# Performance work log

Measured on AMD Instinct MI355X. Metric: run time of the kernel, lower is better.

## Reference

```python
import jax, jax.numpy as jnp
import numpy as np

GRID = 128
N0 = 262144
CHANNELS = [16, 32, 64, 128, 256]
EPS = 1e-5
OFFS2 = [(dx, dy, dz) for dx in (0, 1) for dy in (0, 1) for dz in (0, 1)]
OFFS3 = [(dx, dy, dz) for dx in (-1, 0, 1) for dy in (-1, 0, 1) for dz in (-1, 0, 1)]


def _keys(c, size):
    return (c[:, 0].astype(np.int64) * size + c[:, 1]) * size + c[:, 2]


def _rulebook(in_coords, out_coords, offsets, size_in, stride):
    # explicit-GEMM rulebook: for each kernel offset, (input_idx, output_idx) pairs,
    # padded to n_out with a validity mask so shapes are static.
    ik = _keys(in_coords, size_in)
    order = np.argsort(ik)
    sk = ik[order]
    K, P = len(offsets), out_coords.shape[0]
    I = np.zeros((K, P), np.int32)
    O = np.zeros((K, P), np.int32)
    M = np.zeros((K, P), bool)
    for k, off in enumerate(offsets):
        nbr = out_coords * stride + np.asarray(off)
        valid = np.all((nbr >= 0) & (nbr < size_in), axis=1)
        nk = _keys(np.clip(nbr, 0, size_in - 1), size_in)
        pos = np.minimum(np.searchsorted(sk, nk), len(sk) - 1)
        found = valid & (sk[pos] == nk)
        cnt = int(found.sum())
        I[k, :cnt] = order[pos[found]]
        O[k, :cnt] = np.nonzero(found)[0]
        M[k, :cnt] = True
    return I, O, M


def setup_inputs() -> dict:
    rng = np.random.RandomState(0)
    flat = rng.choice(GRID ** 3, size=N0, replace=False)
    coords = np.stack([flat // (GRID * GRID), (flat // GRID) % GRID, flat % GRID], 1).astype(np.int64)
    key = jax.random.key(0)
    ctr = [0]
    def nrm(shape, scale=1.0):
        ctr[0] += 1
        return scale * jax.random.normal(jax.random.fold_in(key, ctr[0]), shape, jnp.float32)
    inp = {"x": nrm((N0, CHANNELS[0]))}
    size = GRID
    for l in range(4):
        cin, cout = CHANNELS[l], CHANNELS[l + 1]
        out_coords = np.unique(coords // 2, axis=0)
        dI, dO, dM = _rulebook(coords, out_coords, OFFS2, size, 2)       # stride-2, k=2 down conv
        bI, bO, bM = _rulebook(out_coords, out_coords, OFFS3, size // 2, 1)  # stride-1, k=3 block conv
        inp[f"dW{l}"] = nrm((8, cin, cout), (8 * cin) ** -0.5)
        inp[f"dI{l}"] = jnp.asarray(dI); inp[f"dO{l}"] = jnp.asarray(dO); inp[f"dM{l}"] = jnp.asarray(dM)
        inp[f"dG{l}"] = 1.0 + nrm((cout,), 0.1)
        inp[f"dB{l}"] = nrm((cout,), 0.1)
        inp[f"dN{l}"] = int(out_coords.shape[0])
        inp[f"bW{l}"] = nrm((27, cout, cout), (27 * cout) ** -0.5)
        inp[f"bC{l}"] = nrm((cout,), 0.01)
        inp[f"bI{l}"] = jnp.asarray(bI); inp[f"bO{l}"] = jnp.asarray(bO); inp[f"bM{l}"] = jnp.asarray(bM)
        inp[f"bG{l}"] = 1.0 + nrm((cout,), 0.1)
        inp[f"bH{l}"] = nrm((cout,), 0.1)
        coords = out_coords
        size //= 2
    return inp


def _conv(f, W, I, O, M, n_out, bias=None):
    # gather -> GEMM -> scatter-add, one pass per kernel offset (fixed small K)
    out = jnp.zeros((n_out, W.shape[-1]), f.dtype)
    for k in range(W.shape[0]):
        g = jnp.where(M[k][:, None], f[I[k]], 0.0)
        out = out.at[O[k]].add(g @ W[k])
    return out if bias is None else out + bias


def _bn_relu(f, g, b):
    # training-mode BatchNorm over active voxels, fused with ReLU
    m = f.mean(0)
    v = jnp.mean((f - m) ** 2, 0)
    return jax.nn.relu((f - m) * (g * jax.lax.rsqrt(v + EPS)) + b)


def _forward(x, levels):
    outs = [x]
    for (dW, dI, dO, dM, dG, dB, dN, bW, bC, bI, bO, bM, bG, bH) in levels:
        x = _bn_relu(_conv(x, dW, dI, dO, dM, dN), dG, dB)        # down block (bias=False)
        x = _bn_relu(_conv(x, bW, bI, bO, bM, dN, bC), bG, bH)    # ConvBlock
        outs.append(x)
    return tuple(outs)


def reference(x, dW0, dI0, dO0, dM0, dG0, dB0, dN0, bW0, bC0, bI0, bO0, bM0, bG0, bH0,
              dW1, dI1, dO1, dM1, dG1, dB1, dN1, bW1, bC1, bI1, bO1, bM1, bG1, bH1,
              dW2, dI2, dO2, dM2, dG2, dB2, dN2, bW2, bC2, bI2, bO2, bM2, bG2, bH2,
              dW3, dI3, dO3, dM3, dG3, dB3, dN3, bW3, bC3, bI3, bO3, bM3, bG3, bH3):
    levels = [
        (dW0, dI0, dO0, dM0, dG0, dB0, dN0, bW0, bC0, bI0, bO0, bM0, bG0, bH0),
        (dW1, dI1, dO1, dM1, dG1, dB1, dN1, bW1, bC1, bI1, bO1, bM1, bG1, bH1),
        (dW2, dI2, dO2, dM2, dG2, dB2, dN2, bW2, bC2, bI2, bO2, bM2, bG2, bH2),
        (dW3, dI3, dO3, dM3, dG3, dB3, dN3, bW3, bC3, bI3, bO3, bM3, bG3, bH3),
    ]
    return _forward(x, levels)
```

## Files before the change

kernel.cpp:

```cpp
#include <hip/hip_runtime.h>
#include <hip/hip_bf16.h>
#include <stdint.h>
#include <stddef.h>

typedef __hip_bfloat16 bf16;
typedef __attribute__((ext_vector_type(8))) short bf8_t;
typedef __attribute__((ext_vector_type(4))) float f4_t;
static const int CH[5] = {16, 32, 64, 128, 256};

__device__ __forceinline__ float b2f(unsigned short u) {
    return __uint_as_float(((unsigned int)u) << 16);
}
__device__ __forceinline__ unsigned short f2bu(float f) {
    union { bf16 h; unsigned short u; } cv;
    cv.h = __float2bfloat16(f);
    return cv.u;
}
__device__ __forceinline__ void fma4(float4& a, float s, const float4& w) {
    a.x = fmaf(s, w.x, a.x);
    a.y = fmaf(s, w.y, a.y);
    a.z = fmaf(s, w.z, a.z);
    a.w = fmaf(s, w.w, a.w);
}
struct us4 { unsigned short a, b, c, d; };

__global__ void k_sentinel(float* __restrict__ out, float v) {
    if (threadIdx.x == 0) out[0] = v;
}

__global__ void SparseConvEncoder_20633022890309_kernel(
        const unsigned char* __restrict__ bM0, int* __restrict__ flag) {
    if (threadIdx.x == 0) {
        flag[0] = 1;
        flag[1] = 0;
        flag[2] = (bM0[0] == 1 && bM0[1] == 0 && bM0[2] == 0 && bM0[3] == 0 && bM0[4] == 1) ? 1 : 0;
    }
}

__global__ void __launch_bounds__(256) k_copy(const float* __restrict__ x,
                                              float* __restrict__ y, long n) {
    long i = (long)blockIdx.x * 256 + threadIdx.x;
    if (i < n) y[i] = x[i];
}

__global__ void __launch_bounds__(256) k_tob(const float* __restrict__ x,
                                             unsigned short* __restrict__ y, long n) {
    long i = (long)blockIdx.x * 256 + threadIdx.x;
    if (i < n) y[i] = f2bu(x[i]);
}

__global__ void __launch_bounds__(256) k_wt(const float* __restrict__ W,
                                            unsigned short* __restrict__ Wt,
                                            int cin, int cout, long tot) {
    long i = (long)blockIdx.x * 256 + threadIdx.x;
    if (i >= tot) return;
    long cc = (long)cin * cout;
    int k = (int)(i / cc);
    int rem = (int)(i % cc);
    int co = rem / cin, ci = rem % cin;
    Wt[i] = f2bu(W[((long)k * cin + ci) * cout + co]);
}

__global__ void __launch_bounds__(256) k_scatter(const int* __restrict__ I,
                                                 const int* __restrict__ O,
                                                 const void* __restrict__ M,
                                                 const int* __restrict__ flag,
                                                 int* __restrict__ R, int P, int k0, int cnt) {
    int i = blockIdx.x * 256 + threadIdx.x;
    if (i >= cnt) return;
    long gi = (long)k0 * P + i;
    int m = flag[2] ? ((const int*)M)[gi] : (int)((const unsigned char*)M)[gi];
    if (!m) return;
    R[(long)(i / P) * P + O[gi]] = I[gi];
}

__global__ void __launch_bounds__(256) k_init(float* __restrict__ out,
                                              const float* __restrict__ bias,
                                              long total, int maskC) {
    long i = (long)blockIdx.x * 256 + threadIdx.x;
    if (i < total) out[i] = bias ? bias[i & maskC] : 0.f;
}

template <int CIN, int TN, int MODE>
__global__ void __launch_bounds__(256) k_mconv(const unsigned short* __restrict__ Xb,
                                               const unsigned short* __restrict__ Wt,
                                               const float* __restrict__ bias,
                                               const int* __restrict__ R,
                                               float* __restrict__ out,
                                               int n, int cout, int kcnt, int gs) {
    const int lane = threadIdx.x & 63;
    const int wave = threadIdx.x >> 6;
    const int rt = blockIdx.x * 4 + wave;
    const int row_tiles = (n + 15) >> 4;
    if (rt >= row_tiles) return;
    const int m = lane & 15, q = lane >> 4;
    const int o = rt * 16 + m;
    const int co0 = blockIdx.y * (16 * TN);
    const bf8_t zero = {};

    f4_t acc[TN];
#pragma unroll
    for (int t = 0; t < TN; ++t) {
        if (MODE == 0) {
            float bv = bias ? bias[co0 + t * 16 + m] : 0.f;
            acc[t][0] = bv; acc[t][1] = bv; acc[t][2] = bv; acc[t][3] = bv;
        } else if (MODE == 1) {
#pragma unroll
            for (int g = 0; g < 4; ++g) {
                int row = rt * 16 + q * 4 + g;
                acc[t][g] = (row < n) ? out[(long)row * cout + co0 + t * 16 + m] : 0.f;
            }
        } else {
            acc[t][0] = 0.f; acc[t][1] = 0.f; acc[t][2] = 0.f; acc[t][3] = 0.f;
        }
    }

    int ks = 0, ke = kcnt;
    if (MODE == 2) {
        ks = blockIdx.z * gs;
        ke = ks + gs;
        if (ke > kcnt) ke = kcnt;
    }

    bool touched = false;
    for (int kk = ks; kk < ke; ++kk) {
        int r = (o < n) ? R[(long)kk * n + o] : -1;
        if (__ballot(r >= 0) == 0ULL) continue;
        touched = true;
#pragma unroll
        for (int cb = 0; cb < CIN; cb += 32) {
            const bool kval = !(CIN == 16 && q >= 2);
            const int kbase = kval ? (cb + q * 8) : 0;
            long ax = (long)((r >= 0) ? r : 0) * CIN + kbase;
            bf8_t av = *(const bf8_t*)(Xb + ax);
            bf8_t a = (r >= 0 && kval) ? av : zero;
#pragma unroll
            for (int t = 0; t < TN; ++t) {
                int co = co0 + t * 16 + m;
                long bx = ((long)kk * cout + co) * CIN + kbase;
                bf8_t bv = *(const bf8_t*)(Wt + bx);
                bf8_t b = kval ? bv : zero;
                acc[t] = __builtin_amdgcn_mfma_f32_16x16x32_bf16(a, b, acc[t], 0, 0, 0);
            }
        }
    }

    if (MODE == 2 && !touched) return;
#pragma unroll
    for (int t = 0; t < TN; ++t) {
#pragma unroll
        for (int g = 0; g < 4; ++g) {
            int row = rt * 16 + q * 4 + g;
            if (row >= n) continue;
            float* p = out + (long)row * cout + co0 + t * 16 + m;
            if (MODE == 2) atomicAdd(p, acc[t][g]);
            else *p = acc[t][g];
        }
    }
}

static void mconv_dispatch(int cin, int tn, int mode, dim3 grd,
                           const unsigned short* Xb, const unsigned short* Wt,
                           const float* bias, const int* R, float* out,
                           int n, int cout, int kcnt, int gs, hipStream_t stream) {
#define M3_(CC, TT, MM)                                                            \
    if (cin == CC && tn == TT && mode == MM) {                                     \
        k_mconv<CC, TT, MM><<<grd, 256, 0, stream>>>(Xb, Wt, bias, R, out, n,      \
                                                     cout, kcnt, gs);              \
        return;                                                                    \
    }
#define M2_(CC) M3_(CC, 2, 0) M3_(CC, 2, 1) M3_(CC, 2, 2) \
                M3_(CC, 4, 0) M3_(CC, 4, 1) M3_(CC, 4, 2)
    M2_(16) M2_(32) M2_(64) M2_(128) M2_(256)
#undef M2_
#undef M3_
}

static void run_mconv(const unsigned short* Xb, const unsigned short* Wt,
                      const float* bias, const int* I, const int* O, const void* M,
                      const int* flag, int* R, float* out, int n, int cin, int cout,
                      int K, int G, hipStream_t stream) {
    int rt = (n + 15) / 16;
    int bx = (rt + 3) / 4;
    int tn = (cout >= 64) ? 4 : 2;
    int gy = cout / (16 * tn);
    long bxy = (long)bx * gy;
    int kg = 1;
    if (bxy < 512 && G >= K) {
        kg = (int)((1024 + bxy - 1) / bxy);
        if (kg > K) kg = K;
    }
    int gs = (K + kg - 1) / kg;
    kg = (K + gs - 1) / gs;

    if (kg > 1) {
        int cnt = K * n;
        hipMemsetAsync(R, 0xFF, (size_t)cnt * 4, stream);
        k_scatter<<<(cnt + 255) / 256, 256, 0, stream>>>(I, O, M, flag, R, n, 0, cnt);
        long tot = (long)n * cout;
        k_init<<<(int)((tot + 255) / 256), 256, 0, stream>>>(out, bias, tot, cout - 1);
        mconv_dispatch(cin, tn, 2, dim3(bx, gy, kg), Xb, Wt, bias, R, out,
                       n, cout, K, gs, stream);
    } else {
        for (int k0 = 0; k0 < K; k0 += G) {
            int g = (K - k0 < G) ? (K - k0) : G;
            int cnt = g * n;
            hipMemsetAsync(R, 0xFF, (size_t)cnt * 4, stream);
            k_scatter<<<(cnt + 255) / 256, 256, 0, stream>>>(I, O, M, flag, R, n, k0, cnt);
            mconv_dispatch(cin, tn, (k0 == 0) ? 0 : 1, dim3(bx, gy, 1), Xb,
                           Wt + (size_t)k0 * cout * cin, bias, R, out,
                           n, cout, g, g, stream);
        }
    }
}

template <int CIN, int ROWS, int XBF, int MODE>
__global__ void __launch_bounds__(256) k_conv_t(const void* __restrict__ X,
                                                const float* __restrict__ W,
                                                const float* __restrict__ bias,
                                                const int* __restrict__ R,
                                                float* __restrict__ out,
                                                int n, int cout,
                                                int wk0, int kcnt, int gs) {
    const int c4 = threadIdx.x;
    const int by = blockDim.y;
    const int base = blockIdx.x * by * ROWS;
    const float* Xf = (const float*)X;
    const unsigned short* Xb = (const unsigned short*)X;

    int o[ROWS];
    float4 acc[ROWS];
    bool touched[ROWS];
#pragma unroll
    for (int j = 0; j < ROWS; ++j) {
        o[j] = base + j * by + threadIdx.y;
        touched[j] = false;
        acc[j] = make_float4(0.f, 0.f, 0.f, 0.f);
        if (o[j] < n) {
            if (MODE == 0) {
                if (bias) acc[j] = *(const float4*)(bias + c4 * 4);
            } else if (MODE == 1) {
                acc[j] = *(const float4*)(out + (long)o[j] * cout + c4 * 4);
            }
        }
    }
    int ks = 0, ke = kcnt;
    if (MODE == 2) {
        ks = blockIdx.y * gs;
        ke = ks + gs;
        if (ke > kcnt) ke = kcnt;
    }
    for (int kk = ks; kk < ke; ++kk) {
        int r[ROWS];
        bool any = false;
#pragma unroll
        for (int j = 0; j < ROWS; ++j) {
            r[j] = (o[j] < n) ? R[(long)kk * n + o[j]] : -1;
            any = any || (r[j] >= 0);
            touched[j] = touched[j] || (r[j] >= 0);
        }
        if (!any) continue;
        const float* wk = W + ((long)(wk0 + kk) * CIN) * cout + c4 * 4;
#pragma unroll
        for (int ci = 0; ci < CIN; ci += 4) {
            float4 w0 = *(const float4*)(wk + (long)(ci + 0) * cout);
            float4 w1 = *(const float4*)(wk + (long)(ci + 1) * cout);
            float4 w2 = *(const float4*)(wk + (long)(ci + 2) * cout);
            float4 w3 = *(const float4*)(wk + (long)(ci + 3) * cout);
#pragma unroll
            for (int j = 0; j < ROWS; ++j) {
                if (r[j] < 0) continue;
                float x0, x1, x2, x3;
                if (XBF) {
                    us4 u = *(const us4*)(Xb + (long)r[j] * CIN + ci);
                    x0 = b2f(u.a); x1 = b2f(u.b); x2 = b2f(u.c); x3 = b2f(u.d);
                } else {
                    float4 xv = *(const float4*)(Xf + (long)r[j] * CIN + ci);
                    x0 = xv.x; x1 = xv.y; x2 = xv.z; x3 = xv.w;
                }
                fma4(acc[j], x0, w0);
                fma4(acc[j], x1, w1);
                fma4(acc[j], x2, w2);
                fma4(acc[j], x3, w3);
            }
        }
    }
#pragma unroll
    for (int j = 0; j < ROWS; ++j) {
        if (o[j] >= n) continue;
        if (MODE == 2) {
            if (!touched[j]) continue;
            float* p = out + (long)o[j] * cout + c4 * 4;
            atomicAdd(p + 0, acc[j].x);
            atomicAdd(p + 1, acc[j].y);
            atomicAdd(p + 2, acc[j].z);
            atomicAdd(p + 3, acc[j].w);
        } else {
            *(float4*)(out + (long)o[j] * cout + c4 * 4) = acc[j];
        }
    }
}

static void conv_dispatch(int cin, int rows, int xbf, int mode, dim3 grd, dim3 blk,
                          const void* X, const float* W, const float* bias,
                          const int* R, float* out, int n, int cout,
                          int wk0, int kcnt, int gs, hipStream_t stream) {
#define C3_(CC, RR, XB, MM)                                                        \
    if (cin == CC && rows == RR && xbf == XB && mode == MM) {                      \
        k_conv_t<CC, RR, XB, MM><<<grd, blk, 0, stream>>>(X, W, bias, R, out, n,   \
                                                          cout, wk0, kcnt, gs);    \
        return;                                                                    \
    }
#define C2_(CC, RR) C3_(CC, RR, 0, 0) C3_(CC, RR, 0, 1) C3_(CC, RR, 0, 2) \
                    C3_(CC, RR, 1, 0) C3_(CC, RR, 1, 1) C3_(CC, RR, 1, 2)
#define C1_(CC) C2_(CC, 1) C2_(CC, 2) C2_(CC, 4)
    C1_(16) C1_(32) C1_(64) C1_(128) C1_(256)
#undef C1_
#undef C2_
#undef C3_
}

static void run_conv(const void* X, int xbf, const float* W, const float* bias,
                     const int* I, const int* O, const void* M, const int* flag,
                     int* R, float* out, int n, int cin, int cout, int K,
                     int G, hipStream_t stream) {
    int bx = cout / 4, by = 256 / bx;
    int g4 = (n + by * 4 - 1) / (by * 4);
    int g2 = (n + by * 2 - 1) / (by * 2);
    int rows;
    if (g4 >= 1024) rows = 4;
    else if (g2 >= 1024) rows = 2;
    else rows = 1;
    int gridn = (n + by * rows - 1) / (by * rows);
    int kg = 1;
    if (gridn < 768 && G >= K) {
        kg = (2048 + gridn - 1) / gridn;
        if (kg > K) kg = K;
    }
    int gs = (K + kg - 1) / kg;
    kg = (K + gs - 1) / gs;
    dim3 blk(bx, by);
    if (kg > 1) {
        int cnt = K * n;
        hipMemsetAsync(R, 0xFF, (size_t)cnt * 4, stream);
        k_scatter<<<(cnt + 255) / 256, 256, 0, stream>>>(I, O, M, flag, R, n, 0, cnt);
        long tot = (long)n * cout;
        k_init<<<(int)((tot + 255) / 256), 256, 0, stream>>>(out, bias, tot, cout - 1);
        conv_dispatch(cin, rows, xbf, 2, dim3(gridn, kg), blk, X, W, bias, R, out,
                      n, cout, 0, K, gs, stream);
    } else {
        for (int k0 = 0; k0 < K; k0 += G) {
            int g = (K - k0 < G) ? (K - k0) : G;
            int cnt = g * n;
            hipMemsetAsync(R, 0xFF, (size_t)cnt * 4, stream);
            k_scatter<<<(cnt + 255) / 256, 256, 0, stream>>>(I, O, M, flag, R, n, k0, cnt);
            conv_dispatch(cin, rows, xbf, (k0 == 0) ? 0 : 1, dim3(gridn, 1), blk,
                          X, W, bias, R, out, n, cout, k0, g, g, stream);
        }
    }
}

__global__ void __launch_bounds__(256) k_stats(const float* __restrict__ X,
                                               float* __restrict__ sums, int n, int C) {
    int c = threadIdx.x, ty = threadIdx.y, ny = blockDim.y;
    float s1 = 0.f, s2 = 0.f;
    for (int o = blockIdx.x * ny + ty; o < n; o += gridDim.x * ny) {
        float v = X[(long)o * C + c];
        s1 += v;
        s2 += v * v;
    }
    __shared__ float sm[512];
    sm[ty * C + c] = s1;
    sm[256 + ty * C + c] = s2;
    __syncthreads();
    if (ty == 0) {
        for (int t = 1; t < ny; ++t) {
            s1 += sm[t * C + c];
            s2 += sm[256 + t * C + c];
        }
        atomicAdd(&sums[c], s1);
        atomicAdd(&sums[C + c], s2);
    }
}

__global__ void k_final(const float* __restrict__ sums, const float* __restrict__ g,
                        const float* __restrict__ b, float* __restrict__ ss,
                        int n, int C) {
    int c = threadIdx.x;
    if (c >= C) return;
    float inv_n = 1.0f / (float)n;
    float mean = sums[c] * inv_n;
    float var = sums[C + c] * inv_n - mean * mean;
    float sc = g[c] * rsqrtf(var + 1e-5f);
    ss[c] = sc;
    ss[C + c] = b[c] - mean * sc;
}

__global__ void __launch_bounds__(256) k_apply(const float* __restrict__ X,
                                               const float* __restrict__ ss,
                                               void* __restrict__ Y, int ybf,
                                               unsigned short* __restrict__ Y2,
                                               long total, int maskC, int C) {
    long i = (long)blockIdx.x * 256 + threadIdx.x;
    if (i >= total) return;
    int c = (int)(i & (long)maskC);
    float v = fmaf(X[i], ss[c], ss[C + c]);
    v = v > 0.f ? v : 0.f;
    if (ybf) ((unsigned short*)Y)[i] = f2bu(v);
    else     ((float*)Y)[i] = v;
    if (Y2) Y2[i] = f2bu(v);
}

static void run_bn(const float* src, int n, int C, const float* g, const float* b,
                   void* dst, int dst_bf16, unsigned short* dst2,
                   float* sums, float* ss, hipStream_t stream) {
    hipMemsetAsync(sums, 0, 2 * C * sizeof(float), stream);
    dim3 sblk(C, 256 / C);
    int sgrd = (n + (int)sblk.y - 1) / (int)sblk.y;
    if (sgrd > 1024) sgrd = 1024;
    k_stats<<<sgrd, sblk, 0, stream>>>(src, sums, n, C);
    k_final<<<1, C, 0, stream>>>(sums, g, b, ss, n, C);
    long tot = (long)n * C;
    k_apply<<<(int)((tot + 255) / 256), 256, 0, stream>>>(src, ss, dst, dst_bf16,
                                                          dst2, tot, C - 1, C);
}

extern "C" void kernel_launch(void* const* d_in, const int* in_sizes, int n_in,
                              void* d_out, int out_size, void* d_ws, size_t ws_size,
                              hipStream_t stream) {
    float* out = (float*)d_out;

    int stride = 0;
    if (n_in == 57) stride = 14;
    else if (n_in == 53) stride = 13;
    if (!stride) {
        k_sentinel<<<1, 64, 0, stream>>>(out, 10240.f + (float)n_in);
        return;
    }
    static const int o14[13] = {0, 1, 2, 3, 4, 5, 7, 8, 9, 10, 11, 12, 13};
    static const int o13[13] = {0, 1, 2, 3, 4, 5, 6, 7, 8, 9, 10, 11, 12};
    const int* om = (stride == 14) ? o14 : o13;

    long n0 = (long)in_sizes[0];
    int P[4];
    bool ok = (n0 % 16 == 0);
    long total = n0;
    for (int l = 0; l < 4 && ok; ++l) {
        int base = 1 + stride * l;
        int sdI = in_sizes[base + om[1]], sdO = in_sizes[base + om[2]], sdM = in_sizes[base + om[3]];
        int sbI = in_sizes[base + om[8]], sbO = in_sizes[base + om[9]], sbM = in_sizes[base + om[10]];
        if (sdI <= 0 || sdI % 8 != 0 || sdO != sdI || sdM != sdI) { ok = false; break; }
        int p = sdI / 8;
        if (sbI != 27 * p || sbO != sbI || sbM != sbI) { ok = false; break; }
        if (in_sizes[base + om[0]] != 8 * CH[l] * CH[l + 1]) { ok = false; break; }
        if (in_sizes[base + om[6]] != 27 * CH[l + 1] * CH[l + 1]) { ok = false; break; }
        P[l] = p;
        total += (long)p * CH[l + 1];
    }
    if (!ok) {
        k_sentinel<<<1, 64, 0, stream>>>(out, 49152.f);
        return;
    }
    if (total != (long)out_size) {
        k_sentinel<<<1, 64, 0, stream>>>(out, 53248.f);
        return;
    }

    auto al = [](size_t x) { return (x + 255) / 256 * 256; };
    size_t maxBuf = 0, maxP = 0, maxXb = 0;
    long rowsIn[4] = {n0 / 16, P[0], P[1], P[2]};
    for (int l = 0; l < 4; ++l) {
        size_t b = (size_t)P[l] * CH[l + 1];
        if (b > maxBuf) maxBuf = b;
        if ((size_t)P[l] > maxP) maxP = (size_t)P[l];
        size_t xi = (size_t)rowsIn[l] * CH[l];
        if (xi > maxXb) maxXb = xi;
    }
    const size_t fixed = 4096;
    size_t rmin = al(maxP * 4);
    size_t dwt_sz = al((size_t)8 * 128 * 256 * 2);
    size_t bwt_sz = al((size_t)27 * 256 * 256 * 2);
    size_t mf_need = dwt_sz + bwt_sz + al(maxXb * 2) + al(maxBuf * 2) + fixed + rmin;

    if (ws_size >= mf_need) {
        char* wsp = (char*)d_ws;
        unsigned short* dWt = (unsigned short*)wsp; wsp += dwt_sz;
        unsigned short* bWt = (unsigned short*)wsp; wsp += bwt_sz;
        unsigned short* xb = (unsigned short*)wsp;  wsp += al(maxXb * 2);
        unsigned short* bufB = (unsigned short*)wsp; wsp += al(maxBuf * 2);
        float* sums = (float*)wsp; wsp += 1024;
        float* ss = (float*)wsp;   wsp += 1024;
        int* flag = (int*)wsp;     wsp += 2048;
        int* R = (int*)wsp;
        size_t Rbytes = ws_size - (size_t)(wsp - (char*)d_ws);

        SparseConvEncoder_20633022890309_kernel<<<1, 64, 0, stream>>>(
            (const unsigned char*)d_in[1 + om[10]], flag);
        k_copy<<<(int)((n0 + 255) / 256), 256, 0, stream>>>((const float*)d_in[0], out, n0);
        k_tob<<<(int)((n0 + 255) / 256), 256, 0, stream>>>((const float*)d_in[0], xb, n0);

        long coff = n0;
        for (int l = 0; l < 4; ++l) {
            int base = 1 + stride * l;
            const float* dW = (const float*)d_in[base + om[0]];
            const int* dI = (const int*)d_in[base + om[1]];
            const int* dO = (const int*)d_in[base + om[2]];
            const void* dM = d_in[base + om[3]];
            const float* dG = (const float*)d_in[base + om[4]];
            const float* dB = (const float*)d_in[base + om[5]];
            const float* bW = (const float*)d_in[base + om[6]];
            const float* bC = (const float*)d_in[base + om[7]];
            const int* bI = (const int*)d_in[base + om[8]];
            const int* bO = (const int*)d_in[base + om[9]];
            const void* bM = d_in[base + om[10]];
            const float* bG = (const float*)d_in[base + om[11]];
            const float* bH = (const float*)d_in[base + om[12]];
            int n = P[l], cin = CH[l], cout = CH[l + 1];

            int G = (int)(Rbytes / ((size_t)n * 4));
            if (G > 27) G = 27;
            if (G < 1) G = 1;

            float* chunkp = out + coff;

            long dwtot = (long)8 * cin * cout;
            k_wt<<<(int)((dwtot + 255) / 256), 256, 0, stream>>>(dW, dWt, cin, cout, dwtot);
            long bwtot = (long)27 * cout * cout;
            k_wt<<<(int)((bwtot + 255) / 256), 256, 0, stream>>>(bW, bWt, cout, cout, bwtot);

            run_mconv(xb, dWt, nullptr, dI, dO, dM, flag, R, chunkp,
                      n, cin, cout, 8, (G > 8) ? 8 : G, stream);
            run_bn(chunkp, n, cout, dG, dB, bufB, 1, nullptr, sums, ss, stream);

            run_mconv(bufB, bWt, bC, bI, bO, bM, flag, R, chunkp,
                      n, cout, cout, 27, G, stream);
            run_bn(chunkp, n, cout, bG, bH, chunkp, 0,
                   (l < 3) ? xb : nullptr, sums, ss, stream);

            coff += (long)n * cout;
        }
        return;
    }

    int bufB_bf16;
    size_t bufBytes;
    if (ws_size >= fixed + al(maxBuf * 4) + rmin) { bufB_bf16 = 0; bufBytes = al(maxBuf * 4); }
    else if (ws_size >= fixed + al(maxBuf * 2) + rmin) { bufB_bf16 = 1; bufBytes = al(maxBuf * 2); }
    else {
        k_sentinel<<<1, 64, 0, stream>>>(out, 16384.f + (float)(ws_size >> 20));
        return;
    }
    size_t Rbytes = ws_size - fixed - bufBytes;
    char* wsp = (char*)d_ws;
    void* bufB = (void*)wsp;   wsp += bufBytes;
    float* sums = (float*)wsp; wsp += 1024;
    float* ss = (float*)wsp;   wsp += 1024;
    int* flag = (int*)wsp;     wsp += 2048;
    int* R = (int*)wsp;

    SparseConvEncoder_20633022890309_kernel<<<1, 64, 0, stream>>>(
        (const unsigned char*)d_in[1 + om[10]], flag);
    k_copy<<<(int)((n0 + 255) / 256), 256, 0, stream>>>((const float*)d_in[0], out, n0);

    long coff = n0;
    const void* cur_in = d_in[0];
    int cur_xbf = 0;
    for (int l = 0; l < 4; ++l) {
        int base = 1 + stride * l;
        const float* dW = (const float*)d_in[base + om[0]];
        const int* dI = (const int*)d_in[base + om[1]];
        const int* dO = (const int*)d_in[base + om[2]];
        const void* dM = d_in[base + om[3]];
        const float* dG = (const float*)d_in[base + om[4]];
        const float* dB = (const float*)d_in[base + om[5]];
        const float* bW = (const float*)d_in[base + om[6]];
        const float* bC = (const float*)d_in[base + om[7]];
        const int* bI = (const int*)d_in[base + om[8]];
        const int* bO = (const int*)d_in[base + om[9]];
        const void* bM = d_in[base + om[10]];
        const float* bG = (const float*)d_in[base + om[11]];
        const float* bH = (const float*)d_in[base + om[12]];
        int n = P[l], cin = CH[l], cout = CH[l + 1];

        int G = (int)(Rbytes / ((size_t)n * 4));
        if (G > 27) G = 27;
        if (G < 1) G = 1;

        float* chunkp = out + coff;
        run_conv(cur_in, cur_xbf, dW, nullptr, dI, dO, dM, flag, R, chunkp,
                 n, cin, cout, 8, (G > 8) ? 8 : G, stream);
        run_bn(chunkp, n, cout, dG, dB, bufB, bufB_bf16, nullptr, sums, ss, stream);
        run_conv(bufB, bufB_bf16, bW, bC, bI, bO, bM, flag, R, chunkp,
                 n, cout, cout, 27, G, stream);
        run_bn(chunkp, n, cout, bG, bH, chunkp, 0, nullptr, sums, ss, stream);

        cur_in = (const void*)chunkp;
        cur_xbf = 0;
        coff += (long)n * cout;
    }
}
```

Baseline: 867.2 us.

## Specialize sparse conv kernel on full kernel-offset count and fuse small launches

Adds a KT template parameter so that, when all kernel offsets fit in one rulebook chunk, the conv kernel preloads every row index and fully unrolls the offset loop. For CIN=16 it packs two offsets into one 32-wide MFMA instead of zero-padding half the operand. The generic path now batches four rulebook index loads before one ballot. It also fuses the input copy with the bf16 conversion, merges the two weight-transpose launches, and folds the BN finalize kernel into the apply kernel to cut launch count, at the cost of recomputing scale and shift per element and more template instantiations.

```diff
diff --git a/kernel.cpp b/kernel.cpp
--- a/kernel.cpp
+++ b/kernel.cpp
@@ -43,22 +43,37 @@
     if (i < n) y[i] = x[i];
 }
 
-__global__ void __launch_bounds__(256) k_tob(const float* __restrict__ x,
-                                             unsigned short* __restrict__ y, long n) {
+__global__ void __launch_bounds__(256) k_copytob(const float* __restrict__ x,
+                                                 float* __restrict__ y,
+                                                 unsigned short* __restrict__ yb, long n) {
     long i = (long)blockIdx.x * 256 + threadIdx.x;
-    if (i < n) y[i] = f2bu(x[i]);
-}
-
-__global__ void __launch_bounds__(256) k_wt(const float* __restrict__ W,
-                                            unsigned short* __restrict__ Wt,
-                                            int cin, int cout, long tot) {
+    if (i < n) {
+        float v = x[i];
+        y[i] = v;
+        yb[i] = f2bu(v);
+    }
+}
+
+__global__ void __launch_bounds__(256) k_wt2(const float* __restrict__ dW,
+                                             unsigned short* __restrict__ dWt, int dcin,
+                                             const float* __restrict__ bW,
+                                             unsigned short* __restrict__ bWt, int bcin,
+                                             int cout, long dtot, long btot) {
     long i = (long)blockIdx.x * 256 + threadIdx.x;
-    if (i >= tot) return;
-    long cc = (long)cin * cout;
-    int k = (int)(i / cc);
-    int rem = (int)(i % cc);
-    int co = rem / cin, ci = rem % cin;
-    Wt[i] = f2bu(W[((long)k * cin + ci) * cout + co]);
+    if (i < dtot) {
+        long cc = (long)dcin * cout;
+        int k = (int)(i / cc);
+        int rem = (int)(i % cc);
+        int co = rem / dcin, ci = rem % dcin;
+        dWt[i] = f2bu(dW[((long)k * dcin + ci) * cout + co]);
+    } else if (i < dtot + btot) {
+        long j = i - dtot;
+        long cc = (long)bcin * cout;
+        int k = (int)(j / cc);
+        int rem = (int)(j % cc);
+        int co = rem / bcin, ci = rem % bcin;
+        bWt[j] = f2bu(bW[((long)k * bcin + ci) * cout + co]);
+    }
 }
 
 __global__ void __launch_bounds__(256) k_scatter(const int* __restrict__ I,
@@ -81,7 +96,7 @@
     if (i < total) out[i] = bias ? bias[i & maskC] : 0.f;
 }
 
-template <int CIN, int TN, int MODE>
+template <int CIN, int TN, int MODE, int KT>
 __global__ void __launch_bounds__(256) k_mconv(const unsigned short* __restrict__ Xb,
                                                const unsigned short* __restrict__ Wt,
                                                const float* __restrict__ bias,
@@ -115,32 +130,89 @@
         }
     }
 
-    int ks = 0, ke = kcnt;
-    if (MODE == 2) {
-        ks = blockIdx.z * gs;
-        ke = ks + gs;
-        if (ke > kcnt) ke = kcnt;
-    }
-
-    bool touched = false;
-    for (int kk = ks; kk < ke; ++kk) {
-        int r = (o < n) ? R[(long)kk * n + o] : -1;
-        if (__ballot(r >= 0) == 0ULL) continue;
-        touched = true;
-#pragma unroll
-        for (int cb = 0; cb < CIN; cb += 32) {
-            const bool kval = !(CIN == 16 && q >= 2);
-            const int kbase = kval ? (cb + q * 8) : 0;
-            long ax = (long)((r >= 0) ? r : 0) * CIN + kbase;
-            bf8_t av = *(const bf8_t*)(Xb + ax);
-            bf8_t a = (r >= 0 && kval) ? av : zero;
-#pragma unroll
-            for (int t = 0; t < TN; ++t) {
-                int co = co0 + t * 16 + m;
-                long bx = ((long)kk * cout + co) * CIN + kbase;
-                bf8_t bv = *(const bf8_t*)(Wt + bx);
-                bf8_t b = kval ? bv : zero;
-                acc[t] = __builtin_amdgcn_mfma_f32_16x16x32_bf16(a, b, acc[t], 0, 0, 0);
+    bool touched = (MODE != 2);
+
+    if constexpr (KT > 0) {
+        int r[KT];
+#pragma unroll
+        for (int kk = 0; kk < KT; ++kk)
+            r[kk] = (o < n) ? R[(long)kk * n + o] : -1;
+
+        if constexpr (CIN == 16) {
+#pragma unroll
+            for (int p = 0; p < KT / 2; ++p) {
+                int rsel = (q < 2) ? r[2 * p] : r[2 * p + 1];
+                long ax = (long)((rsel >= 0) ? rsel : 0) * CIN + (q & 1) * 8;
+                bf8_t av = *(const bf8_t*)(Xb + ax);
+                bf8_t a = (rsel >= 0) ? av : zero;
+                int ksel = 2 * p + (q >> 1);
+#pragma unroll
+                for (int t = 0; t < TN; ++t) {
+                    int co = co0 + t * 16 + m;
+                    long bx = ((long)ksel * cout + co) * CIN + (q & 1) * 8;
+                    bf8_t b = *(const bf8_t*)(Wt + bx);
+                    acc[t] = __builtin_amdgcn_mfma_f32_16x16x32_bf16(a, b, acc[t], 0, 0, 0);
+                }
+            }
+        } else {
+#pragma unroll
+            for (int kk = 0; kk < KT; ++kk) {
+#pragma unroll
+                for (int cb = 0; cb < CIN; cb += 32) {
+                    long ax = (long)((r[kk] >= 0) ? r[kk] : 0) * CIN + cb + q * 8;
+                    bf8_t av = *(const bf8_t*)(Xb + ax);
+                    bf8_t a = (r[kk] >= 0) ? av : zero;
+#pragma unroll
+                    for (int t = 0; t < TN; ++t) {
+                        int co = co0 + t * 16 + m;
+                        long bx = ((long)kk * cout + co) * CIN + cb + q * 8;
+                        bf8_t b = *(const bf8_t*)(Wt + bx);
+                        acc[t] = __builtin_amdgcn_mfma_f32_16x16x32_bf16(a, b, acc[t], 0, 0, 0);
+                    }
+                }
+            }
+        }
+    } else {
+        int ks = 0, ke = kcnt;
+        if (MODE == 2) {
+            ks = blockIdx.z * gs;
+            ke = ks + gs;
+            if (ke > kcnt) ke = kcnt;
+        }
+        for (int kb = ks; kb < ke; kb += 4) {
+            int r4[4];
+#pragma unroll
+            for (int j = 0; j < 4; ++j) {
+                int kk = kb + j;
+                r4[j] = (kk < ke && o < n) ? R[(long)kk * n + o] : -1;
+            }
+            if (MODE == 2) {
+                unsigned long long bl =
+                    __ballot((r4[0] >= 0) | (r4[1] >= 0) | (r4[2] >= 0) | (r4[3] >= 0));
+                if (bl == 0ULL) continue;
+                touched = true;
+            }
+#pragma unroll
+            for (int j = 0; j < 4; ++j) {
+                int kk = kb + j;
+                if (kk >= ke) break;
+                int r = r4[j];
+#pragma unroll
+                for (int cb = 0; cb < CIN; cb += 32) {
+                    const bool kval = !(CIN == 16 && q >= 2);
+                    const int kbase = kval ? (cb + q * 8) : 0;
+                    long ax = (long)((r >= 0) ? r : 0) * CIN + kbase;
+                    bf8_t av = *(const bf8_t*)(Xb + ax);
+                    bf8_t a = (r >= 0 && kval) ? av : zero;
+#pragma unroll
+                    for (int t = 0; t < TN; ++t) {
+                        int co = co0 + t * 16 + m;
+                        long bx = ((long)kk * cout + co) * CIN + kbase;
+                        bf8_t bv = *(const bf8_t*)(Wt + bx);
+                        bf8_t b = kval ? bv : zero;
+                        acc[t] = __builtin_amdgcn_mfma_f32_16x16x32_bf16(a, b, acc[t], 0, 0, 0);
+                    }
+                }
             }
         }
     }
@@ -159,14 +231,22 @@
     }
 }
 
-static void mconv_dispatch(int cin, int tn, int mode, dim3 grd,
+static void mconv_dispatch(int cin, int tn, int mode, int kt, dim3 grd,
                            const unsigned short* Xb, const unsigned short* Wt,
                            const float* bias, const int* R, float* out,
                            int n, int cout, int kcnt, int gs, hipStream_t stream) {
+#define MF_(CC, TT, KK)                                                            \
+    if (cin == CC && tn == TT && mode == 0 && kt == KK) {                          \
+        k_mconv<CC, TT, 0, KK><<<grd, 256, 0, stream>>>(Xb, Wt, bias, R, out, n,   \
+                                                        cout, kcnt, gs);           \
+        return;                                                                    \
+    }
+    MF_(16, 2, 8) MF_(32, 4, 8) MF_(32, 2, 27) MF_(64, 4, 27)
+#undef MF_
 #define M3_(CC, TT, MM)                                                            \
     if (cin == CC && tn == TT && mode == MM) {                                     \
-        k_mconv<CC, TT, MM><<<grd, 256, 0, stream>>>(Xb, Wt, bias, R, out, n,      \
-                                                     cout, kcnt, gs);              \
+        k_mconv<CC, TT, MM, 0><<<grd, 256, 0, stream>>>(Xb, Wt, bias, R, out, n,   \
+                                                        cout, kcnt, gs);           \
         return;                                                                    \
     }
 #define M2_(CC) M3_(CC, 2, 0) M3_(CC, 2, 1) M3_(CC, 2, 2) \
@@ -199,7 +279,7 @@
         k_scatter<<<(cnt + 255) / 256, 256, 0, stream>>>(I, O, M, flag, R, n, 0, cnt);
         long tot = (long)n * cout;
         k_init<<<(int)((tot + 255) / 256), 256, 0, stream>>>(out, bias, tot, cout - 1);
-        mconv_dispatch(cin, tn, 2, dim3(bx, gy, kg), Xb, Wt, bias, R, out,
+        mconv_dispatch(cin, tn, 2, 0, dim3(bx, gy, kg), Xb, Wt, bias, R, out,
                        n, cout, K, gs, stream);
     } else {
         for (int k0 = 0; k0 < K; k0 += G) {
@@ -207,7 +287,8 @@
             int cnt = g * n;
             hipMemsetAsync(R, 0xFF, (size_t)cnt * 4, stream);
             k_scatter<<<(cnt + 255) / 256, 256, 0, stream>>>(I, O, M, flag, R, n, k0, cnt);
-            mconv_dispatch(cin, tn, (k0 == 0) ? 0 : 1, dim3(bx, gy, 1), Xb,
+            int kt = (k0 == 0 && g == K) ? K : 0;
+            mconv_dispatch(cin, tn, (k0 == 0) ? 0 : 1, kt, dim3(bx, gy, 1), Xb,
                            Wt + (size_t)k0 * cout * cin, bias, R, out,
                            n, cout, g, g, stream);
         }
@@ -383,28 +464,21 @@
     }
 }
 
-__global__ void k_final(const float* __restrict__ sums, const float* __restrict__ g,
-                        const float* __restrict__ b, float* __restrict__ ss,
-                        int n, int C) {
-    int c = threadIdx.x;
-    if (c >= C) return;
-    float inv_n = 1.0f / (float)n;
-    float mean = sums[c] * inv_n;
-    float var = sums[C + c] * inv_n - mean * mean;
-    float sc = g[c] * rsqrtf(var + 1e-5f);
-    ss[c] = sc;
-    ss[C + c] = b[c] - mean * sc;
-}
-
 __global__ void __launch_bounds__(256) k_apply(const float* __restrict__ X,
-                                               const float* __restrict__ ss,
+                                               const float* __restrict__ sums,
+                                               const float* __restrict__ g,
+                                               const float* __restrict__ b,
                                                void* __restrict__ Y, int ybf,
                                                unsigned short* __restrict__ Y2,
-                                               long total, int maskC, int C) {
+                                               long total, int maskC, int C, float inv_n) {
     long i = (long)blockIdx.x * 256 + threadIdx.x;
     if (i >= total) return;
     int c = (int)(i & (long)maskC);
-    float v = fmaf(X[i], ss[c], ss[C + c]);
+    float mean = sums[c] * inv_n;
+    float var = fmaf(-mean, mean, sums[C + c] * inv_n);
+    float sc = g[c] * rsqrtf(var + 1e-5f);
+    float sh = fmaf(-mean, sc, b[c]);
+    float v = fmaf(X[i], sc, sh);
     v = v > 0.f ? v : 0.f;
     if (ybf) ((unsigned short*)Y)[i] = f2bu(v);
     else     ((float*)Y)[i] = v;
@@ -413,16 +487,16 @@
 
 static void run_bn(const float* src, int n, int C, const float* g, const float* b,
                    void* dst, int dst_bf16, unsigned short* dst2,
-                   float* sums, float* ss, hipStream_t stream) {
+                   float* sums, hipStream_t stream) {
     hipMemsetAsync(sums, 0, 2 * C * sizeof(float), stream);
     dim3 sblk(C, 256 / C);
     int sgrd = (n + (int)sblk.y - 1) / (int)sblk.y;
     if (sgrd > 1024) sgrd = 1024;
     k_stats<<<sgrd, sblk, 0, stream>>>(src, sums, n, C);
-    k_final<<<1, C, 0, stream>>>(sums, g, b, ss, n, C);
     long tot = (long)n * C;
-    k_apply<<<(int)((tot + 255) / 256), 256, 0, stream>>>(src, ss, dst, dst_bf16,
-                                                          dst2, tot, C - 1, C);
+    k_apply<<<(int)((tot + 255) / 256), 256, 0, stream>>>(src, sums, g, b, dst, dst_bf16,
+                                                          dst2, tot, C - 1, C,
+                                                          1.0f / (float)n);
 }
 
 extern "C" void kernel_launch(void* const* d_in, const int* in_sizes, int n_in,
@@ -489,15 +563,14 @@
         unsigned short* xb = (unsigned short*)wsp;  wsp += al(maxXb * 2);
         unsigned short* bufB = (unsigned short*)wsp; wsp += al(maxBuf * 2);
         float* sums = (float*)wsp; wsp += 1024;
-        float* ss = (float*)wsp;   wsp += 1024;
         int* flag = (int*)wsp;     wsp += 2048;
         int* R = (int*)wsp;
         size_t Rbytes = ws_size - (size_t)(wsp - (char*)d_ws);
 
         SparseConvEncoder_20633022890309_kernel<<<1, 64, 0, stream>>>(
             (const unsigned char*)d_in[1 + om[10]], flag);
-        k_copy<<<(int)((n0 + 255) / 256), 256, 0, stream>>>((const float*)d_in[0], out, n0);
-        k_tob<<<(int)((n0 + 255) / 256), 256, 0, stream>>>((const float*)d_in[0], xb, n0);
+        k_copytob<<<(int)((n0 + 255) / 256), 256, 0, stream>>>((const float*)d_in[0],
+                                                               out, xb, n0);
 
         long coff = n0;
         for (int l = 0; l < 4; ++l) {
@@ -524,18 +597,18 @@
             float* chunkp = out + coff;
 
             long dwtot = (long)8 * cin * cout;
-            k_wt<<<(int)((dwtot + 255) / 256), 256, 0, stream>>>(dW, dWt, cin, cout, dwtot);
             long bwtot = (long)27 * cout * cout;
-            k_wt<<<(int)((bwtot + 255) / 256), 256, 0, stream>>>(bW, bWt, cout, cout, bwtot);
+            k_wt2<<<(int)((dwtot + bwtot + 255) / 256), 256, 0, stream>>>(
+                dW, dWt, cin, bW, bWt, cout, cout, dwtot, bwtot);
 
             run_mconv(xb, dWt, nullptr, dI, dO, dM, flag, R, chunkp,
                       n, cin, cout, 8, (G > 8) ? 8 : G, stream);
-            run_bn(chunkp, n, cout, dG, dB, bufB, 1, nullptr, sums, ss, stream);
+            run_bn(chunkp, n, cout, dG, dB, bufB, 1, nullptr, sums, stream);
 
             run_mconv(bufB, bWt, bC, bI, bO, bM, flag, R, chunkp,
                       n, cout, cout, 27, G, stream);
             run_bn(chunkp, n, cout, bG, bH, chunkp, 0,
-                   (l < 3) ? xb : nullptr, sums, ss, stream);
+                   (l < 3) ? xb : nullptr, sums, stream);
 
             coff += (long)n * cout;
         }
@@ -554,7 +627,6 @@
     char* wsp = (char*)d_ws;
     void* bufB = (void*)wsp;   wsp += bufBytes;
     float* sums = (float*)wsp; wsp += 1024;
-    float* ss = (float*)wsp;   wsp += 1024;
     int* flag = (int*)wsp;     wsp += 2048;
     int* R = (int*)wsp;
 
@@ -589,10 +661,10 @@
         float* chunkp = out + coff;
         run_conv(cur_in, cur_xbf, dW, nullptr, dI, dO, dM, flag, R, chunkp,
                  n, cin, cout, 8, (G > 8) ? 8 : G, stream);
-        run_bn(chunkp, n, cout, dG, dB, bufB, bufB_bf16, nullptr, sums, ss, stream);
+        run_bn(chunkp, n, cout, dG, dB, bufB, bufB_bf16, nullptr, sums, stream);
         run_conv(bufB, bufB_bf16, bW, bC, bI, bO, bM, flag, R, chunkp,
                  n, cout, cout, 27, G, stream);
-        run_bn(chunkp, n, cout, bG, bH, chunkp, 0, nullptr, sums, ss, stream);
+        run_bn(chunkp, n, cout, bG, bH, chunkp, 0, nullptr, sums, stream);
 
         cur_in = (const void*)chunkp;
         cur_xbf = 0;
```

Result: faster. 830.3 us (-4.3%).
